# Kernel optimization log

Hardware: AMD Instinct MI355X
Metric: run time of the kernel (lower is better)

## Reference

```python
import jax, jax.numpy as jnp
import numpy as np

N_TOKENS = 8192
NQ = 6
NL = 2


def ry_mat(theta):
    # theta: scalar or (B,) -> (2,2) or (B,2,2) complex RY matrix
    c = jnp.cos(theta / 2)
    s = jnp.sin(theta / 2)
    return jnp.stack([jnp.stack([c, -s], -1), jnp.stack([s, c], -1)], -2).astype(jnp.complex64)


def apply_1q(state, gate, q, nq):
    # state: (B, 2**nq); gate: (2,2) shared or (B,2,2) per-batch
    B = state.shape[0]
    st = state.reshape(B, 2 ** q, 2, -1)
    if gate.ndim == 3:
        st = jnp.einsum('bij,bajc->baic', gate, st)
    else:
        st = jnp.einsum('ij,bajc->baic', gate, st)
    return st.reshape(B, -1)


def apply_rz(state, theta, q, nq):
    # diagonal RZ: multiply phases, no matmul needed
    B = state.shape[0]
    st = state.reshape(B, 2 ** q, 2, -1)
    ph = jnp.stack([jnp.exp(-0.5j * theta), jnp.exp(0.5j * theta)]).astype(jnp.complex64)
    return (st * ph[None, None, :, None]).reshape(B, -1)


def apply_cnot(state, c, t, nq):
    B = state.shape[0]
    st = state.reshape((B,) + (2,) * nq)
    s0 = jnp.take(st, 0, axis=1 + c)
    s1 = jnp.take(st, 1, axis=1 + c)
    ta = 1 + t - (1 if t > c else 0)  # target axis after removing control axis
    s1 = jnp.flip(s1, axis=ta)
    st = jnp.stack([s0, s1], axis=1 + c)
    return st.reshape(B, -1)


def prepare_states(x, params, nl, nq):
    # x: (B, nq) angles; params: (nl, nq, 2). Returns (B, 2**nq) complex statevectors.
    B = x.shape[0]
    state = jnp.zeros((B, 2 ** nq), jnp.complex64).at[:, 0].set(1.0)
    for q in range(nq):  # RY angle embedding
        state = apply_1q(state, ry_mat(x[:, q]), q, nq)
    for l in range(nl):  # PQC layers: RY, RZ rotations + CNOT ring
        for q in range(nq):
            state = apply_1q(state, ry_mat(params[l, q, 0]), q, nq)
            state = apply_rz(state, params[l, q, 1], q, nq)
        for q in range(nq):
            state = apply_cnot(state, q, (q + 1) % nq, nq)
    return state


def setup_inputs() -> dict:
    key = jax.random.key(0)
    k1, k2, k3, k4 = jax.random.split(key, 4)
    return {
        'x_tokens': jax.random.normal(k1, (N_TOKENS, NQ), dtype=jnp.float32),
        'params_q': 0.1 * jax.random.normal(k2, (NL, NQ, 2), dtype=jnp.float32),
        'params_k': 0.1 * jax.random.normal(k3, (NL, NQ, 2), dtype=jnp.float32),
        'params_v': 0.1 * jax.random.normal(k4, (NL, NQ, 2), dtype=jnp.float32),
    }


def reference(x_tokens, params_q, params_k, params_v):
    nq = x_tokens.shape[1]
    nl = params_q.shape[0]
    sq = prepare_states(x_tokens, params_q, nl, nq)  # (N, 2**nq)
    sk = prepare_states(x_tokens, params_k, nl, nq)
    ov = jnp.einsum('id,jd->ij', sq, jnp.conj(sk))  # pairwise overlaps (N, N)
    logits = jnp.real(ov * jnp.conj(ov))            # swap-test fidelity |<q|k>|^2
    attn = jax.nn.softmax(logits, axis=-1)
    sv = prepare_states(x_tokens, params_v, nl, nq)
    probs = jnp.real(sv * jnp.conj(sv))             # (N, 2**nq)
    idx = jnp.arange(2 ** nq)
    bits = (idx[None, :] >> (nq - 1 - jnp.arange(nq))[:, None]) & 1  # (nq, 2**nq)
    signs = (1.0 - 2.0 * bits).astype(probs.dtype)
    V = probs @ signs.T                              # <Z_q> per qubit -> (N, nq)
    return attn @ V
```

## Files before the change

### kernel.cpp

```cpp
#include <hip/hip_runtime.h>
#include <hip/hip_bf16.h>
#include <hip/hip_fp16.h>

#define NT 8192
#define NQB 6
#define NL 2
#define JSPLIT 16
#define JSLICE (NT / JSPLIT)
#define CHUNK 32
#define NCHUNK (JSLICE / CHUNK)
#define IPW 32
#define WPB 4
#define IPB (IPW * WPB)
#define NBI (NT / IPB)
#define WSTRIDE 40

typedef _Float16 f16x8 __attribute__((ext_vector_type(8)));
typedef float f32x4 __attribute__((ext_vector_type(4)));

static __device__ __forceinline__ unsigned int pack_h2(float a, float b) {
  unsigned short lo = __builtin_bit_cast(unsigned short, (_Float16)a);
  unsigned short hi = __builtin_bit_cast(unsigned short, (_Float16)b);
  return (unsigned int)lo | ((unsigned int)hi << 16);
}

static __device__ __forceinline__ unsigned int pkrtz(float a, float b) {
  return __builtin_bit_cast(unsigned int, __builtin_amdgcn_cvt_pkrtz(a, b));
}

static __device__ __forceinline__ int cnot_src(int p, int q) {
  const int mc = 1 << (5 - q);
  const int mt = 1 << (5 - ((q + 1) % NQB));
  return (p & mc) ? (p ^ mt) : p;
}

#define GLOAD_LDS16(g, l)                                      \
  __builtin_amdgcn_global_load_lds(                            \
      (const __attribute__((address_space(1))) void*)(g),      \
      (__attribute__((address_space(3))) void*)(l), 16, 0, 0)

__global__ __launch_bounds__(256) void prep_kernel(
    const float* __restrict__ x, const float* __restrict__ pq,
    const float* __restrict__ pk, const float* __restrict__ pv,
    unsigned int* __restrict__ Are, unsigned int* __restrict__ Bk,
    unsigned short* __restrict__ Vt)
{
  const int wid  = blockIdx.x * 4 + (threadIdx.x >> 6);
  const int lane = threadIdx.x & 63;
  const int set  = wid >> 13;
  const int tok  = wid & (NT - 1);
  const float* pp = (set == 0) ? pq : ((set == 1) ? pk : pv);

  int m = lane;
#pragma unroll
  for (int q = 5; q >= 0; --q) m = cnot_src(m, q);
  int inv = lane;
#pragma unroll
  for (int q = 0; q < 6; ++q) inv = cnot_src(inv, q);

  float a = 0.f;
  if (lane < 6)                    a = 0.5f * x[tok * NQB + lane];
  else if (lane >= 8 && lane < 14) a = 0.5f * pp[(lane - 8) * 2];
  else if (lane >= 16 && lane < 22) a = 0.5f * pp[12 + (lane - 16) * 2];
  float sa, ca;
  __sincosf(a, &sa, &ca);

  float R = 1.f;
#pragma unroll
  for (int q = 0; q < 6; ++q) {
    const float tqs = __shfl(sa, q, 64),     tqc = __shfl(ca, q, 64);
    const float prs = __shfl(sa, 8 + q, 64), prc = __shfl(ca, 8 + q, 64);
    const float s = tqs * prc + tqc * prs;
    const float c = tqc * prc - tqs * prs;
    R *= ((m >> (5 - q)) & 1) ? s : c;
  }
  float phi0 = 0.f;
#pragma unroll
  for (int q = 0; q < 6; ++q) {
    const float bh = 0.5f * pp[q * 2 + 1];
    phi0 += ((m >> (5 - q)) & 1) ? bh : -bh;
  }
  float s0, c0;
  __sincosf(phi0, &s0, &c0);
  float re = R * c0, im = R * s0;

#pragma unroll
  for (int q = 0; q < 6; ++q) {
    const int mask = 1 << (5 - q);
    const float rcs = __shfl(sa, 16 + q, 64), rcc = __shfl(ca, 16 + q, 64);
    const float pre = __shfl_xor(re, mask, 64);
    const float pim = __shfl_xor(im, mask, 64);
    const float se = (lane & mask) ? rcs : -rcs;
    re = fmaf(se, pre, rcc * re);
    im = fmaf(se, pim, rcc * im);
  }
  float phi1 = 0.f;
#pragma unroll
  for (int q = 0; q < 6; ++q) {
    const float bh = 0.5f * pp[12 + q * 2 + 1];
    phi1 += ((lane >> (5 - q)) & 1) ? bh : -bh;
  }
  float s1, c1;
  __sincosf(phi1, &s1, &c1);
  const float fre = re * c1 - im * s1;
  const float fim = re * s1 + im * c1;

  if (set == 0) {
    Are[tok * 64 + inv] = pack_h2(fre, fim);
  } else if (set == 1) {
    const int sidx = ((((inv >> 2) ^ (tok & 15)) << 2) | (inv & 3));
    Bk[tok * 64 + sidx] = pack_h2(fre, fim);
  } else {
    const float prob = fre * fre + fim * fim;
    float vq[NQB];
#pragma unroll
    for (int q = 0; q < NQB; ++q) {
      float v = (inv & (1 << (5 - q))) ? -prob : prob;
#pragma unroll
      for (int off = 1; off < 64; off <<= 1) v += __shfl_xor(v, off, 64);
      vq[q] = v;
    }
    if (lane < 16) {
      const int q = lane & 7;
      float sel = vq[0];
      if (q == 1) sel = vq[1];
      if (q == 2) sel = vq[2];
      if (q == 3) sel = vq[3];
      if (q == 4) sel = vq[4];
      if (q == 5) sel = vq[5];
      if (q == 6) sel = 1.0f;
      if (q == 7) sel = 0.0f;
      float outv;
      if (lane < 8) {
        outv = sel;
      } else {
        const float hi = (float)(_Float16)sel;
        outv = (q < 6) ? (sel - hi) : 0.0f;
      }
      Vt[lane * NT + tok] = __builtin_bit_cast(unsigned short, (_Float16)outv);
    }
  }
}

__global__ __launch_bounds__(256, 2) void attn_kernel(
    const uint4* __restrict__ Are, const uint4* __restrict__ Bk,
    const unsigned short* __restrict__ Vt, float* __restrict__ part)
{
  __shared__ uint4 kbuf[2][CHUNK * 16];
  __shared__ __align__(16) unsigned short wbuf[2][WPB][2][16][WSTRIDE];

  const int tid  = threadIdx.x;
  const int lane = tid & 63;
  const int wave = tid >> 6;
  const int col  = lane & 15;
  const int quad = lane >> 4;

  const int ib = blockIdx.x & (NBI - 1);
  const int js = blockIdx.x >> 6;
  const int ibase = ib * IPB + wave * IPW;
  const int jbase0 = js * JSLICE;

  f16x8 qRe[2][4];
#pragma unroll
  for (int rt = 0; rt < 2; ++rt) {
    const uint4* pr = Are + (ibase + rt * 16 + col) * 16 + quad;
#pragma unroll
    for (int s = 0; s < 4; ++s) qRe[rt][s] = __builtin_bit_cast(f16x8, pr[s * 4]);
  }

  int koff[4];
#pragma unroll
  for (int s = 0; s < 4; ++s) koff[s] = (((s * 4 + quad) ^ col) << 4);

  f32x4 acc[2] = {{0.f, 0.f, 0.f, 0.f}, {0.f, 0.f, 0.f, 0.f}};

  auto stage = [&](int buf, int c) {
#pragma unroll
    for (int r = 0; r < 2; ++r) {
      const int slot = wave * 2 + r;
      GLOAD_LDS16(Bk + (size_t)(jbase0 + c * CHUNK) * 16 + slot * 64 + lane,
                  &kbuf[buf][slot * 64]);
    }
  };

  stage(0, 0);
  asm volatile("s_waitcnt vmcnt(0)" ::: "memory");
  __builtin_amdgcn_s_barrier();
  asm volatile("" ::: "memory");

  f16x8 vb_prev;
#pragma unroll 1
  for (int c = 0; c < NCHUNK; ++c) {
    const int cur = c & 1;
    const int jb = jbase0 + c * CHUNK;
    if (c + 1 < NCHUNK) stage(cur ^ 1, c + 1);
    const f16x8 vb = *(const f16x8*)(Vt + (size_t)col * NT + jb + quad * 8);
    f16x8 wA0, wA1;
    if (c > 0) {
      wA0 = *(const f16x8*)&wbuf[cur ^ 1][wave][0][col][quad * 8];
      wA1 = *(const f16x8*)&wbuf[cur ^ 1][wave][1][col][quad * 8];
    }

#pragma unroll
    for (int ct = 0; ct < 2; ++ct) {
      const char* kb = (const char*)kbuf[cur] + (ct * 16 + col) * 256;
      f16x8 bfr[4], bfi[4];
#pragma unroll
      for (int s = 0; s < 4; ++s) {
        const uint4 u = *(const uint4*)(kb + koff[s]);
        uint4 w;
        w.x = ((u.x << 16) | (u.x >> 16)) ^ 0x00008000u;
        w.y = ((u.y << 16) | (u.y >> 16)) ^ 0x00008000u;
        w.z = ((u.z << 16) | (u.z >> 16)) ^ 0x00008000u;
        w.w = ((u.w << 16) | (u.w >> 16)) ^ 0x00008000u;
        bfr[s] = __builtin_bit_cast(f16x8, u);
        bfi[s] = __builtin_bit_cast(f16x8, w);
      }
#pragma unroll
      for (int rt = 0; rt < 2; ++rt) {
        f32x4 aR = {0.f, 0.f, 0.f, 0.f};
        f32x4 aI = {0.f, 0.f, 0.f, 0.f};
#pragma unroll
        for (int s = 0; s < 4; ++s) {
          aR = __builtin_amdgcn_mfma_f32_16x16x32_f16(bfr[s], qRe[rt][s], aR, 0, 0, 0);
          aI = __builtin_amdgcn_mfma_f32_16x16x32_f16(bfi[s], qRe[rt][s], aI, 0, 0, 0);
        }
        const float w0 = __expf(aR[0] * aR[0] + aI[0] * aI[0]);
        const float w1 = __expf(aR[1] * aR[1] + aI[1] * aI[1]);
        const float w2 = __expf(aR[2] * aR[2] + aI[2] * aI[2]);
        const float w3 = __expf(aR[3] * aR[3] + aI[3] * aI[3]);
        *(uint2*)&wbuf[cur][wave][rt][col][ct * 16 + quad * 4] =
            make_uint2(pkrtz(w0, w1), pkrtz(w2, w3));
      }
    }
    if (c > 0) {
      acc[0] = __builtin_amdgcn_mfma_f32_16x16x32_f16(wA0, vb_prev, acc[0], 0, 0, 0);
      acc[1] = __builtin_amdgcn_mfma_f32_16x16x32_f16(wA1, vb_prev, acc[1], 0, 0, 0);
    }
    vb_prev = vb;

    if (c + 1 < NCHUNK) {
      asm volatile("s_waitcnt vmcnt(0)" ::: "memory");
      __builtin_amdgcn_s_barrier();
      asm volatile("" ::: "memory");
    }
  }
  {
    const int cur = (NCHUNK - 1) & 1;
    const f16x8 wA0 = *(const f16x8*)&wbuf[cur][wave][0][col][quad * 8];
    const f16x8 wA1 = *(const f16x8*)&wbuf[cur][wave][1][col][quad * 8];
    acc[0] = __builtin_amdgcn_mfma_f32_16x16x32_f16(wA0, vb_prev, acc[0], 0, 0, 0);
    acc[1] = __builtin_amdgcn_mfma_f32_16x16x32_f16(wA1, vb_prev, acc[1], 0, 0, 0);
  }

#pragma unroll
  for (int rt = 0; rt < 2; ++rt) {
    float res[4];
#pragma unroll
    for (int r = 0; r < 4; ++r) res[r] = acc[rt][r] + __shfl_xor(acc[rt][r], 8, 64);
    if (col < 8) {
      float* p = part + ((size_t)(js * NT + ibase + rt * 16 + quad * 4)) * 8 + col;
#pragma unroll
      for (int r = 0; r < 4; ++r) p[r * 8] = res[r];
    }
  }
}

__global__ __launch_bounds__(256) void combine_kernel(
    const float* __restrict__ part, float* __restrict__ out)
{
  const int row = blockIdx.x * 256 + threadIdx.x;
  float acc[7] = {0.f, 0.f, 0.f, 0.f, 0.f, 0.f, 0.f};
#pragma unroll
  for (int js = 0; js < JSPLIT; ++js) {
    const float* p = part + ((size_t)(js * NT + row)) * 8;
#pragma unroll
    for (int q = 0; q < 7; ++q) acc[q] += p[q];
  }
  const float inv = 1.0f / acc[6];
#pragma unroll
  for (int q = 0; q < 6; ++q)
    out[row * 6 + q] = acc[q] * inv;
}

extern "C" void kernel_launch(void* const* d_in, const int* in_sizes, int n_in,
                              void* d_out, int out_size, void* d_ws, size_t ws_size,
                              hipStream_t stream) {
  const float* x  = (const float*)d_in[0];
  const float* pq = (const float*)d_in[1];
  const float* pk = (const float*)d_in[2];
  const float* pv = (const float*)d_in[3];
  char* ws = (char*)d_ws;
  unsigned int*   Are = (unsigned int*)(ws);
  unsigned int*   Bk  = (unsigned int*)(ws + (size_t)(2u << 20));
  unsigned short* Vt  = (unsigned short*)(ws + (size_t)(4u << 20));
  float*          prt = (float*)(ws + (size_t)(4u << 20) + (size_t)(256u << 10));

  prep_kernel<<<(NT * 3) / 4, 256, 0, stream>>>(x, pq, pk, pv, Are, Bk, Vt);
  attn_kernel<<<NBI * JSPLIT, 256, 0, stream>>>((const uint4*)Are, (const uint4*)Bk,
                                                Vt, prt);
  combine_kernel<<<NT / 256, 256, 0, stream>>>(prt, (float*)d_out);
}
```

Before: 135.0 us.

## Triple-buffer key chunks, precompute imaginary Q fragments, and drop deferred PV stage

Staging of key chunks becomes a three-buffer ring with prefetch two chunks ahead and partial vmcnt waits, so global-to-LDS loads get more time to land before each barrier. The imaginary-part operand is now built once from the Q registers instead of swizzling every K fragment read from LDS each iteration, which removes per-chunk ALU work. The PV MFMA is now done in the same iteration rather than software-pipelined with a double-buffered weight tile, and s_setprio wraps the QK MFMAs. The cost is more LDS for the third K buffer, more registers for qIm, and a possible RAW stall on wbuf within the iteration without an explicit barrier.

```diff
diff --git a/kernel.cpp b/kernel.cpp
--- a/kernel.cpp
+++ b/kernel.cpp
@@ -146,8 +146,8 @@
     const uint4* __restrict__ Are, const uint4* __restrict__ Bk,
     const unsigned short* __restrict__ Vt, float* __restrict__ part)
 {
-  __shared__ uint4 kbuf[2][CHUNK * 16];
-  __shared__ __align__(16) unsigned short wbuf[2][WPB][2][16][WSTRIDE];
+  __shared__ uint4 kbuf[3][CHUNK * 16];
+  __shared__ __align__(16) unsigned short wbuf[WPB][2][16][WSTRIDE];
 
   const int tid  = threadIdx.x;
   const int lane = tid & 63;
@@ -160,12 +160,21 @@
   const int ibase = ib * IPB + wave * IPW;
   const int jbase0 = js * JSLICE;
 
-  f16x8 qRe[2][4];
+  f16x8 qRe[2][4], qIm[2][4];
 #pragma unroll
   for (int rt = 0; rt < 2; ++rt) {
     const uint4* pr = Are + (ibase + rt * 16 + col) * 16 + quad;
 #pragma unroll
-    for (int s = 0; s < 4; ++s) qRe[rt][s] = __builtin_bit_cast(f16x8, pr[s * 4]);
+    for (int s = 0; s < 4; ++s) {
+      const uint4 u = pr[s * 4];
+      uint4 w;
+      w.x = ((u.x << 16) | (u.x >> 16)) ^ 0x80000000u;
+      w.y = ((u.y << 16) | (u.y >> 16)) ^ 0x80000000u;
+      w.z = ((u.z << 16) | (u.z >> 16)) ^ 0x80000000u;
+      w.w = ((u.w << 16) | (u.w >> 16)) ^ 0x80000000u;
+      qRe[rt][s] = __builtin_bit_cast(f16x8, u);
+      qIm[rt][s] = __builtin_bit_cast(f16x8, w);
+    }
   }
 
   int koff[4];
@@ -174,83 +183,70 @@
 
   f32x4 acc[2] = {{0.f, 0.f, 0.f, 0.f}, {0.f, 0.f, 0.f, 0.f}};
 
+  const uint4* sbase = Bk + (size_t)jbase0 * 16 + (size_t)(wave * 2) * 64 + lane;
   auto stage = [&](int buf, int c) {
-#pragma unroll
-    for (int r = 0; r < 2; ++r) {
-      const int slot = wave * 2 + r;
-      GLOAD_LDS16(Bk + (size_t)(jbase0 + c * CHUNK) * 16 + slot * 64 + lane,
-                  &kbuf[buf][slot * 64]);
-    }
+    const uint4* src = sbase + (size_t)c * (CHUNK * 16);
+    GLOAD_LDS16(src,      &kbuf[buf][(wave * 2 + 0) * 64]);
+    GLOAD_LDS16(src + 64, &kbuf[buf][(wave * 2 + 1) * 64]);
   };
 
   stage(0, 0);
-  asm volatile("s_waitcnt vmcnt(0)" ::: "memory");
+  __builtin_amdgcn_sched_barrier(0);
+  stage(1, 1);
+  asm volatile("s_waitcnt vmcnt(2)" ::: "memory");
   __builtin_amdgcn_s_barrier();
   asm volatile("" ::: "memory");
 
-  f16x8 vb_prev;
+  const unsigned short* vtp = Vt + (size_t)col * NT + jbase0 + quad * 8;
+
+  int cur = 0;
 #pragma unroll 1
   for (int c = 0; c < NCHUNK; ++c) {
-    const int cur = c & 1;
-    const int jb = jbase0 + c * CHUNK;
-    if (c + 1 < NCHUNK) stage(cur ^ 1, c + 1);
-    const f16x8 vb = *(const f16x8*)(Vt + (size_t)col * NT + jb + quad * 8);
-    f16x8 wA0, wA1;
-    if (c > 0) {
-      wA0 = *(const f16x8*)&wbuf[cur ^ 1][wave][0][col][quad * 8];
-      wA1 = *(const f16x8*)&wbuf[cur ^ 1][wave][1][col][quad * 8];
-    }
+    if (c + 2 < NCHUNK) {
+      int nb = cur + 2; if (nb >= 3) nb -= 3;
+      stage(nb, c + 2);
+    }
+    const f16x8 vb = *(const f16x8*)(vtp + c * CHUNK);
 
 #pragma unroll
     for (int ct = 0; ct < 2; ++ct) {
       const char* kb = (const char*)kbuf[cur] + (ct * 16 + col) * 256;
-      f16x8 bfr[4], bfi[4];
-#pragma unroll
-      for (int s = 0; s < 4; ++s) {
-        const uint4 u = *(const uint4*)(kb + koff[s]);
-        uint4 w;
-        w.x = ((u.x << 16) | (u.x >> 16)) ^ 0x00008000u;
-        w.y = ((u.y << 16) | (u.y >> 16)) ^ 0x00008000u;
-        w.z = ((u.z << 16) | (u.z >> 16)) ^ 0x00008000u;
-        w.w = ((u.w << 16) | (u.w >> 16)) ^ 0x00008000u;
-        bfr[s] = __builtin_bit_cast(f16x8, u);
-        bfi[s] = __builtin_bit_cast(f16x8, w);
-      }
+      f16x8 bfr[4];
+#pragma unroll
+      for (int s = 0; s < 4; ++s) bfr[s] = *(const f16x8*)(kb + koff[s]);
 #pragma unroll
       for (int rt = 0; rt < 2; ++rt) {
         f32x4 aR = {0.f, 0.f, 0.f, 0.f};
         f32x4 aI = {0.f, 0.f, 0.f, 0.f};
+        __builtin_amdgcn_s_setprio(1);
 #pragma unroll
         for (int s = 0; s < 4; ++s) {
           aR = __builtin_amdgcn_mfma_f32_16x16x32_f16(bfr[s], qRe[rt][s], aR, 0, 0, 0);
-          aI = __builtin_amdgcn_mfma_f32_16x16x32_f16(bfi[s], qRe[rt][s], aI, 0, 0, 0);
+          aI = __builtin_amdgcn_mfma_f32_16x16x32_f16(bfr[s], qIm[rt][s], aI, 0, 0, 0);
         }
+        __builtin_amdgcn_s_setprio(0);
         const float w0 = __expf(aR[0] * aR[0] + aI[0] * aI[0]);
         const float w1 = __expf(aR[1] * aR[1] + aI[1] * aI[1]);
         const float w2 = __expf(aR[2] * aR[2] + aI[2] * aI[2]);
         const float w3 = __expf(aR[3] * aR[3] + aI[3] * aI[3]);
-        *(uint2*)&wbuf[cur][wave][rt][col][ct * 16 + quad * 4] =
+        *(uint2*)&wbuf[wave][rt][col][ct * 16 + quad * 4] =
             make_uint2(pkrtz(w0, w1), pkrtz(w2, w3));
       }
     }
-    if (c > 0) {
-      acc[0] = __builtin_amdgcn_mfma_f32_16x16x32_f16(wA0, vb_prev, acc[0], 0, 0, 0);
-      acc[1] = __builtin_amdgcn_mfma_f32_16x16x32_f16(wA1, vb_prev, acc[1], 0, 0, 0);
-    }
-    vb_prev = vb;
+    {
+      const f16x8 wA0 = *(const f16x8*)&wbuf[wave][0][col][quad * 8];
+      const f16x8 wA1 = *(const f16x8*)&wbuf[wave][1][col][quad * 8];
+      acc[0] = __builtin_amdgcn_mfma_f32_16x16x32_f16(wA0, vb, acc[0], 0, 0, 0);
+      acc[1] = __builtin_amdgcn_mfma_f32_16x16x32_f16(wA1, vb, acc[1], 0, 0, 0);
+    }
 
     if (c + 1 < NCHUNK) {
-      asm volatile("s_waitcnt vmcnt(0)" ::: "memory");
+      if (c + 2 < NCHUNK) asm volatile("s_waitcnt vmcnt(2)" ::: "memory");
+      else                asm volatile("s_waitcnt vmcnt(0)" ::: "memory");
       __builtin_amdgcn_s_barrier();
       asm volatile("" ::: "memory");
     }
-  }
-  {
-    const int cur = (NCHUNK - 1) & 1;
-    const f16x8 wA0 = *(const f16x8*)&wbuf[cur][wave][0][col][quad * 8];
-    const f16x8 wA1 = *(const f16x8*)&wbuf[cur][wave][1][col][quad * 8];
-    acc[0] = __builtin_amdgcn_mfma_f32_16x16x32_f16(wA0, vb_prev, acc[0], 0, 0, 0);
-    acc[1] = __builtin_amdgcn_mfma_f32_16x16x32_f16(wA1, vb_prev, acc[1], 0, 0, 0);
+    cur = (cur + 1 == 3) ? 0 : cur + 1;
   }
 
 #pragma unroll
```

Result: slower. 143.6 us (+6.3%).
